# Kernel tuning notes

Measured on AMD Instinct MI355X. Metric: run time of the kernel, lower is better.

The kernel has to match this reference:

```python
import jax, jax.numpy as jnp
import numpy as np

B, L, D, H = 2, 2048, 1024, 16
Dh = D // H  # 64


def setup_inputs() -> dict:
    key = jax.random.key(0)
    ks = jax.random.split(key, 5)
    s_in = 1.0 / np.sqrt(D).astype(np.float32)
    s_out = 1.0 / np.sqrt(H * Dh).astype(np.float32)
    x = jax.random.normal(ks[0], (B, L, D), dtype=jnp.float32)
    Wq = jax.random.normal(ks[1], (D, H, Dh), dtype=jnp.float32) * s_in
    Wk = jax.random.normal(ks[2], (D, H, Dh), dtype=jnp.float32) * s_in
    Wv = jax.random.normal(ks[3], (D, H, Dh), dtype=jnp.float32) * s_in
    Wo = jax.random.normal(ks[4], (H, Dh, D), dtype=jnp.float32) * s_out
    bq = jnp.zeros((H, Dh), dtype=jnp.float32)
    bk = jnp.zeros((H, Dh), dtype=jnp.float32)
    bv = jnp.zeros((H, Dh), dtype=jnp.float32)
    bo = jnp.zeros((D,), dtype=jnp.float32)
    return {"x": x, "Wq": Wq, "bq": bq, "Wk": Wk, "bk": bk, "Wv": Wv, "bv": bv, "Wo": Wo, "bo": bo}


def reference(x, Wq, bq, Wk, bk, Wv, bv, Wo, bo):
    # QKV projections: LinearGeneral in_features=D -> (H, Dh), with bias
    q = jnp.einsum('bld,dhk->blhk', x, Wq) + bq  # [B,L,H,Dh]
    k = jnp.einsum('bld,dhk->blhk', x, Wk) + bk
    v = jnp.einsum('bld,dhk->blhk', x, Wv) + bv
    # NOTE: source uses FLOOR division for the scale (q // Dh**0.5) -- replicate exactly.
    q = q // (Dh ** 0.5)
    attn = jnp.einsum('blhk,bnhk->bhln', q, k)  # [B,H,L,L]
    causal = jnp.tril(jnp.ones((1, 1, L, L), dtype=jnp.float32))  # bidir=False -> pure causal
    neg_inf = jnp.finfo(jnp.float32).min
    attn = jnp.where(causal > 0, attn, neg_inf)
    attn = jax.nn.softmax(attn, axis=-1)
    o = jnp.einsum('bhln,bnhk->blhk', attn, v)  # [B,L,H,Dh]
    # Output projection: LinearGeneral (H, Dh) -> D over axes (-2,-1), with bias
    return jnp.einsum('blhk,hkd->bld', o, Wo) + bo
```

## Files before the change

kernel.cpp:

```cpp
#include <hip/hip_runtime.h>
#include <cstddef>
#include <cstdint>
#include <math.h>

typedef __bf16 bf16_t;
typedef __bf16 bf16x8 __attribute__((ext_vector_type(8)));
typedef float  f32x4  __attribute__((ext_vector_type(4)));

#define MFMA16(A,B,C) __builtin_amdgcn_mfma_f32_16x16x32_bf16((A),(B),(C),0,0,0)
#define QFIX_CAP 262144
#define QWIN 2e-3f


__device__ __forceinline__ void gload16(const bf16_t* g, bf16_t* l)
{
    auto* lp = reinterpret_cast<__attribute__((address_space(3))) uint32_t*>(
                   reinterpret_cast<uintptr_t>(l));
    const auto* gp = reinterpret_cast<const __attribute__((address_space(1))) uint32_t*>(
                   reinterpret_cast<uintptr_t>(g));
    __builtin_amdgcn_global_load_lds(gp, lp, 16, 0, 0);
}

__device__ __forceinline__ void gload4(const float* g, float* l)
{
    auto* lp = reinterpret_cast<__attribute__((address_space(3))) uint32_t*>(
                   reinterpret_cast<uintptr_t>(l));
    const auto* gp = reinterpret_cast<const __attribute__((address_space(1))) uint32_t*>(
                   reinterpret_cast<uintptr_t>(g));
    __builtin_amdgcn_global_load_lds(gp, lp, 4, 0, 0);
}

__global__ void k_conv_x(const float* __restrict__ x, bf16_t* __restrict__ xhi)
{
    int i = blockIdx.x * blockDim.x + threadIdx.x;
    float4 v = reinterpret_cast<const float4*>(x)[i];
    bf16_t* ph = xhi + 4*(size_t)i;
    ph[0]=(bf16_t)v.x; ph[1]=(bf16_t)v.y; ph[2]=(bf16_t)v.z; ph[3]=(bf16_t)v.w;
}

__global__ void k_transpose(const float* __restrict__ W, bf16_t* __restrict__ T)
{
    __shared__ float tile[32][33];
    int t = threadIdx.x, r = t >> 5, c = t & 31;
    int k0 = blockIdx.y * 32, n0 = blockIdx.x * 32;
#pragma unroll
    for (int i = 0; i < 4; i++)
        tile[r + i*8][c] = W[(size_t)(k0 + r + i*8) * 1024 + n0 + c];
    __syncthreads();
#pragma unroll
    for (int i = 0; i < 4; i++) {
        int nr = r + i*8;
        T[(size_t)(n0 + nr) * 1024 + k0 + c] = (bf16_t)tile[c][nr];
    }
}

__global__ void k_transpose_f32(const float* __restrict__ W, float* __restrict__ T)
{
    __shared__ float tile[32][33];
    int t = threadIdx.x, r = t >> 5, c = t & 31;
    int k0 = blockIdx.y * 32, n0 = blockIdx.x * 32;
#pragma unroll
    for (int i = 0; i < 4; i++)
        tile[r + i*8][c] = W[(size_t)(k0 + r + i*8) * 1024 + n0 + c];
    __syncthreads();
#pragma unroll
    for (int i = 0; i < 4; i++) {
        int nr = r + i*8;
        T[(size_t)(n0 + nr) * 1024 + k0 + c] = tile[c][nr];
    }
}

template<int MODE>
__launch_bounds__(256)
__global__ void k_gemm3(const bf16_t* __restrict__ A, const bf16_t* __restrict__ Bt,
                        const float* __restrict__ b0, const float* __restrict__ b1,
                        const float* __restrict__ b2,
                        bf16_t* __restrict__ qout, int2* __restrict__ qwl,
                        int* __restrict__ qcnt,
                        bf16_t* __restrict__ kho, bf16_t* __restrict__ vho,
                        float* __restrict__ fout)
{
    constexpr int BM = (MODE == 0) ? 128 : 64;
    __shared__ bf16_t As[3][BM*32]  __attribute__((aligned(16)));
    __shared__ bf16_t Bs[3][128*32] __attribute__((aligned(16)));

    const int bid = blockIdx.x;
    const int xcd = bid & 7;
    const int i   = bid >> 3;
    int n0, m0;
    if constexpr (MODE == 0) {
        n0 = (xcd * 3 + (i % 3)) * 128;
        m0 = (i / 3) * 128;
    } else {
        n0 = xcd * 128;
        m0 = i * 64;
    }

    const int tid = threadIdx.x;
    const int wid = tid >> 6, lane = tid & 63, lane16 = lane & 15, lg = lane >> 4;
    constexpr int WM = (MODE == 0) ? 64 : 32;
    const int wm = (wid >> 1) * WM, wn = (wid & 1) * 64;
    constexpr int MI = (MODE == 0) ? 4 : 2;

    f32x4 acc[MI][4] = {};

    auto STAGE = [&](int buf, int kt) {
        const int k0 = kt * 32;
#pragma unroll
        for (int i2 = 0; i2 < BM/64; i2++) {
            const int c = tid + i2*256;
            const int row = c >> 2, col = (c & 3) * 8;
            gload16(&A[(size_t)(m0 + row) * 1024 + k0 + col], &As[buf][c*8]);
        }
#pragma unroll
        for (int i2 = 0; i2 < 2; i2++) {
            const int c = tid + i2*256;
            const int row = c >> 2, col = (c & 3) * 8;
            gload16(&Bt[(size_t)(n0 + row) * 1024 + k0 + col], &Bs[buf][c*8]);
        }
    };

    STAGE(0, 0);
    STAGE(1, 1);
    for (int kt = 0; kt < 32; ++kt) {
        const int cur = kt % 3;
        if (kt < 31) {
            if constexpr (MODE == 0) { asm volatile("s_waitcnt vmcnt(4)" ::: "memory"); }
            else                     { asm volatile("s_waitcnt vmcnt(3)" ::: "memory"); }
        } else asm volatile("s_waitcnt vmcnt(0)" ::: "memory");
        __builtin_amdgcn_s_barrier();

        bf16x8 a[MI], b[4];
#pragma unroll
        for (int ii = 0; ii < MI; ii++)
            a[ii] = *reinterpret_cast<const bf16x8*>(&As[cur][(wm + ii*16 + lane16)*32 + lg*8]);
#pragma unroll
        for (int j = 0; j < 4; j++)
            b[j] = *reinterpret_cast<const bf16x8*>(&Bs[cur][(wn + j*16 + lane16)*32 + lg*8]);
#pragma unroll
        for (int ii = 0; ii < MI; ii++)
#pragma unroll
            for (int j = 0; j < 4; j++)
                acc[ii][j] = MFMA16(a[ii], b[j], acc[ii][j]);

        if (kt + 2 < 32) STAGE((kt + 2) % 3, kt + 2);
    }

    if constexpr (MODE == 1) {
#pragma unroll
        for (int j = 0; j < 4; j++) {
            const int n = n0 + wn + j*16 + lane16;
#pragma unroll
            for (int ii = 0; ii < MI; ii++)
#pragma unroll
                for (int r = 0; r < 4; r++) {
                    const int m = m0 + wm + ii*16 + lg*4 + r;
                    fout[(size_t)m*1024 + n] = acc[ii][j][r] + b0[n];
                }
        }
    } else if (n0 >= 1024) {
#pragma unroll
        for (int j = 0; j < 4; j++) {
            const int n = n0 + wn + j*16 + lane16;
#pragma unroll
            for (int ii = 0; ii < MI; ii++)
#pragma unroll
                for (int r = 0; r < 4; r++) {
                    const int m = m0 + wm + ii*16 + lg*4 + r;
                    const int bb = m >> 11, l = m & 2047;
                    float v = acc[ii][j][r];
                    if (n < 2048) {
                        const int nk = n - 1024;
                        kho[(((size_t)(bb*16 + (nk>>6)))*2048 + l)*64 + (nk&63)] =
                            (bf16_t)(v + b1[nk]);
                    } else {
                        const int nv = n - 2048;
                        vho[(((size_t)(bb*16 + (nv>>6)))*64 + (nv&63))*2048 + l] =
                            (bf16_t)(v + b2[nv]);
                    }
                }
        }
    } else {
        int cnt = 0;
#pragma unroll
        for (int j = 0; j < 4; j++) {
            const int n = n0 + wn + j*16 + lane16;
            const float bias = b0[n];
#pragma unroll
            for (int ii = 0; ii < MI; ii++)
#pragma unroll
                for (int r = 0; r < 4; r++) {
                    const int m = m0 + wm + ii*16 + lg*4 + r;
                    const int bb = m >> 11, l = m & 2047;
                    float t  = (acc[ii][j][r] + bias) * 0.125f;
                    float fl = floorf(t);
                    float fr = t - fl;
                    cnt += (fr < QWIN || fr > 1.0f - QWIN) ? 1 : 0;
                    qout[(((size_t)(bb*16 + (n>>6)))*2048 + l)*64 + (n&63)] = (bf16_t)fl;
                }
        }
        int pre = cnt;
#pragma unroll
        for (int off = 1; off < 64; off <<= 1) {
            int t2 = __shfl_up(pre, off);
            if (lane >= off) pre += t2;
        }
        int total = __shfl(pre, 63);
        int base = 0;
        if (lane == 63 && total > 0) base = atomicAdd(qcnt, total);
        base = __shfl(base, 63);
        int idx = base + pre - cnt;
#pragma unroll
        for (int j = 0; j < 4; j++) {
            const int n = n0 + wn + j*16 + lane16;
            const float bias = b0[n];
#pragma unroll
            for (int ii = 0; ii < MI; ii++)
#pragma unroll
                for (int r = 0; r < 4; r++) {
                    const int m = m0 + wm + ii*16 + lg*4 + r;
                    float t  = (acc[ii][j][r] + bias) * 0.125f;
                    float fr = t - floorf(t);
                    if (fr < QWIN || fr > 1.0f - QWIN) {
                        if (idx < QFIX_CAP) qwl[idx] = make_int2(m, n);
                        idx++;
                    }
                }
        }
    }
}

__launch_bounds__(64)
__global__ void k_qfix(const float* __restrict__ x, const float* __restrict__ WqT,
                       const float* __restrict__ bq, const int2* __restrict__ wl,
                       const int* __restrict__ count, bf16_t* __restrict__ qout)
{
    __shared__ float xs [64][65];
    __shared__ float wsd[64][65];
    int cnt = *count; if (cnt > QFIX_CAP) cnt = QFIX_CAP;
    const int base = blockIdx.x * 64;
    if (base >= cnt) return;
    const int lane = threadIdx.x;
    const int i = base + lane;
    const bool act = (i < cnt);
    const int2 e = wl[act ? i : base];
    const int m = e.x, n = e.y;

    float r0 = 0.f, r1 = 0.f;
#pragma unroll 1
    for (int c = 0; c < 16; ++c) {
        const int d0 = c * 64;
#pragma unroll 8
        for (int s = 0; s < 64; ++s) {
            int ms = __shfl(m, s);
            int ns = __shfl(n, s);
            gload4(&x  [(size_t)ms * 1024 + d0 + lane], &xs [s][0]);
            gload4(&WqT[(size_t)ns * 1024 + d0 + lane], &wsd[s][0]);
        }
        asm volatile("s_waitcnt vmcnt(0)" ::: "memory");
        float racc = (c < 8) ? r0 : r1;
#pragma unroll
        for (int d = 0; d < 64; ++d)
            racc = fmaf(xs[lane][d], wsd[lane][d], racc);
        if (c < 8) r0 = racc; else r1 = racc;
        asm volatile("s_waitcnt lgkmcnt(0)" ::: "memory");
    }
    if (act) {
        float acc = __fadd_rn(r0, r1);
        float q = floorf(__fmul_rn(__fadd_rn(acc, bq[n]), 0.125f));
        qout[(((size_t)((m>>11)*16 + (n>>6)))*2048 + (m&2047))*64 + (n&63)] = (bf16_t)q;
    }
}

__launch_bounds__(256)
__global__ void k_attn(const bf16_t* __restrict__ qf,
                       const bf16_t* __restrict__ khi,
                       const bf16_t* __restrict__ vhiT,
                       bf16_t* __restrict__ ohi)
{
    __shared__ bf16_t Kh[2][64*72] __attribute__((aligned(16)));
    __shared__ bf16_t Vh[2][64*72] __attribute__((aligned(16)));
    __shared__ bf16_t Ph[4*16*72]  __attribute__((aligned(16)));
    const int tid = threadIdx.x, wid = tid >> 6, lane = tid & 63;
    const int lane16 = lane & 15, lg = lane >> 4;
    const int bid = blockIdx.x;
    const int xcd = bid & 7;
    const int ib  = bid >> 3;
    const int bh  = xcd * 4 + (ib & 3);
    const int bx  = ib >> 2;
    const bf16_t* qb  = qf   + (size_t)bh * 2048 * 64;
    const bf16_t* khb = khi  + (size_t)bh * 2048 * 64;
    const bf16_t* vhb = vhiT + (size_t)bh * 64 * 2048;
    const int b = bh >> 4, h = bh & 15;
    const float L2E = 1.44269504088896f;

    bf16x8 kreg[2], vreg[2];
    auto ISSUE = [&](int t) {
        const int kv0 = t * 64;
#pragma unroll
        for (int i = 0; i < 2; i++) {
            int cc = tid + i*256, row = cc >> 3, col8 = (cc & 7) * 8;
            kreg[i] = *reinterpret_cast<const bf16x8*>(&khb[(size_t)(kv0+row)*64 + col8]);
            vreg[i] = *reinterpret_cast<const bf16x8*>(&vhb[(size_t)row*2048 + kv0 + col8]);
        }
    };
    auto WRITE = [&](int buf) {
#pragma unroll
        for (int i = 0; i < 2; i++) {
            int cc = tid + i*256, row = cc >> 3, col8 = (cc & 7) * 8;
            *reinterpret_cast<bf16x8*>(&Kh[buf][row*72 + col8]) = kreg[i];
            *reinterpret_cast<bf16x8*>(&Vh[buf][row*72 + col8]) = vreg[i];
        }
    };

#pragma unroll 1
    for (int pass = 0; pass < 2; pass++) {
        const int qt = pass ? (31 - bx) : bx;
        const int q0 = qt * 64;
        const int qrow16 = q0 + wid*16 + lane16;

        bf16x8 qfr0 = *reinterpret_cast<const bf16x8*>(&qb[(size_t)qrow16*64 + lg*8]);
        bf16x8 qfr1 = *reinterpret_cast<const bf16x8*>(&qb[(size_t)qrow16*64 + 32 + lg*8]);

        f32x4 acco[4] = {};
        float mrow = -1e30f;
        float lrow[4] = {0.f, 0.f, 0.f, 0.f};

        __syncthreads();
        ISSUE(0);
        WRITE(0);

        for (int t = 0; t <= qt; t++) {
            const int cur = t & 1;
            if (t < qt) ISSUE(t + 1);
            __syncthreads();

            f32x4 s[4] = {};
            __builtin_amdgcn_s_setprio(1);
#pragma unroll
            for (int st = 0; st < 4; st++) {
                const int ro = (st*16 + lane16)*72;
                bf16x8 kh0 = *reinterpret_cast<const bf16x8*>(&Kh[cur][ro + lg*8]);
                bf16x8 kh1 = *reinterpret_cast<const bf16x8*>(&Kh[cur][ro + 32 + lg*8]);
                s[st] = MFMA16(qfr0, kh0, s[st]);
                s[st] = MFMA16(qfr1, kh1, s[st]);
            }
            __builtin_amdgcn_s_setprio(0);
            if (t == qt) {
#pragma unroll
                for (int st = 0; st < 4; st++) {
                    int key = t*64 + st*16 + lane16;
#pragma unroll
                    for (int r = 0; r < 4; r++) {
                        int qr = q0 + wid*16 + lg*4 + r;
                        if (key > qr) s[st][r] = -1e30f;
                    }
                }
            }
            float gm = s[0][0];
#pragma unroll
            for (int st = 0; st < 4; st++)
#pragma unroll
                for (int r = 0; r < 4; r++) gm = fmaxf(gm, s[st][r]);
#pragma unroll
            for (int off = 1; off < 16; off <<= 1)
                gm = fmaxf(gm, __shfl_xor(gm, off));

            if (__any(gm > mrow)) {
                float mn = fmaxf(mrow, gm);
                float scl = exp2f((mrow - mn) * L2E);
                mrow = mn;
#pragma unroll
                for (int r = 0; r < 4; r++) lrow[r] *= scl;
#pragma unroll
                for (int nf = 0; nf < 4; nf++)
#pragma unroll
                    for (int r = 0; r < 4; r++) acco[nf][r] *= scl;
            }
#pragma unroll
            for (int st = 0; st < 4; st++) {
#pragma unroll
                for (int r = 0; r < 4; r++) {
                    float p = exp2f((s[st][r] - mrow) * L2E);
                    lrow[r] += p;
                    Ph[wid*16*72 + (lg*4 + r)*72 + st*16 + lane16] = (bf16_t)p;
                }
            }

            __builtin_amdgcn_s_setprio(1);
#pragma unroll
            for (int ks = 0; ks < 2; ks++) {
                bf16x8 phf = *reinterpret_cast<const bf16x8*>(&Ph[wid*16*72 + lane16*72 + ks*32 + lg*8]);
#pragma unroll
                for (int nf = 0; nf < 4; nf++) {
                    bf16x8 vh = *reinterpret_cast<const bf16x8*>(&Vh[cur][(nf*16 + lane16)*72 + ks*32 + lg*8]);
                    acco[nf] = MFMA16(phf, vh, acco[nf]);
                }
            }
            __builtin_amdgcn_s_setprio(0);

            if (t < qt) WRITE(cur ^ 1);
        }

#pragma unroll
        for (int off = 1; off < 16; off <<= 1)
#pragma unroll
            for (int r = 0; r < 4; r++) lrow[r] += __shfl_xor(lrow[r], off);

#pragma unroll
        for (int r = 0; r < 4; r++) {
            float inv = 1.0f / lrow[r];
            int qr = q0 + wid*16 + lg*4 + r;
            size_t base = ((size_t)(b*2048 + qr))*1024 + h*64;
#pragma unroll
            for (int nf = 0; nf < 4; nf++)
                ohi[base + nf*16 + lane16] = (bf16_t)(acco[nf][r] * inv);
        }
    }
}

extern "C" void kernel_launch(void* const* d_in, const int* in_sizes, int n_in,
                              void* d_out, int out_size, void* d_ws, size_t ws_size,
                              hipStream_t stream)
{
    const float* x  = (const float*)d_in[0];
    const float* Wq = (const float*)d_in[1];
    const float* bq = (const float*)d_in[2];
    const float* Wk = (const float*)d_in[3];
    const float* bk = (const float*)d_in[4];
    const float* Wv = (const float*)d_in[5];
    const float* bv = (const float*)d_in[6];
    const float* Wo = (const float*)d_in[7];
    const float* bo = (const float*)d_in[8];

    char* ws = (char*)d_ws;
    const size_t MB = (size_t)1 << 20;
    bf16_t* xhi    = (bf16_t*)(ws +  0*MB);
    bf16_t* WThi   = (bf16_t*)(ws +  8*MB);
    bf16_t* WoThi  = (bf16_t*)(ws + 14*MB);
    bf16_t* qbuf   = (bf16_t*)(ws + 16*MB);
    bf16_t* khibuf = (bf16_t*)(ws + 24*MB);
    bf16_t* vhiT   = (bf16_t*)(ws + 32*MB);
    bf16_t* ohibuf = (bf16_t*)(ws + 40*MB);
    int2*   qwl    = (int2*)  (ws + 48*MB);
    int*    qcnt   = (int*)   (ws + 50*MB);
    float*  WqTf   = (float*) (ws + 52*MB);

    hipMemsetAsync(qcnt, 0, 4, stream);
    k_conv_x<<<4096, 256, 0, stream>>>(x, xhi);
    dim3 tg(32, 32);
    k_transpose<<<tg, 256, 0, stream>>>(Wq, WThi);
    k_transpose<<<tg, 256, 0, stream>>>(Wk, WThi + (size_t)1024*1024);
    k_transpose<<<tg, 256, 0, stream>>>(Wv, WThi + (size_t)2048*1024);
    k_transpose<<<tg, 256, 0, stream>>>(Wo, WoThi);
    k_transpose_f32<<<tg, 256, 0, stream>>>(Wq, WqTf);

    k_gemm3<0><<<768, 256, 0, stream>>>(xhi, WThi, bq, bk, bv,
                                        qbuf, qwl, qcnt, khibuf, vhiT, nullptr);
    k_qfix<<<4096, 64, 0, stream>>>(x, WqTf, bq, qwl, qcnt, qbuf);
    k_attn<<<512, 256, 0, stream>>>(qbuf, khibuf, vhiT, ohibuf);
    k_gemm3<1><<<512, 256, 0, stream>>>(ohibuf, WoThi, bo, nullptr, nullptr,
                                        nullptr, nullptr, nullptr,
                                        nullptr, nullptr, (float*)d_out);
}
```

Before: 239.3 us.

## Switch GEMM to double-buffered BK=64 pipeline and 128-row output tiles

```diff
diff --git a/kernel.cpp b/kernel.cpp
--- a/kernel.cpp
+++ b/kernel.cpp
@@ -80,9 +80,8 @@
                         bf16_t* __restrict__ kho, bf16_t* __restrict__ vho,
                         float* __restrict__ fout)
 {
-    constexpr int BM = (MODE == 0) ? 128 : 64;
-    __shared__ bf16_t As[3][BM*32]  __attribute__((aligned(16)));
-    __shared__ bf16_t Bs[3][128*32] __attribute__((aligned(16)));
+    __shared__ bf16_t As[2][128*64] __attribute__((aligned(16)));
+    __shared__ bf16_t Bs[2][128*64] __attribute__((aligned(16)));
 
     const int bid = blockIdx.x;
     const int xcd = bid & 7;
@@ -93,57 +92,58 @@
         m0 = (i / 3) * 128;
     } else {
         n0 = xcd * 128;
-        m0 = i * 64;
+        m0 = i * 128;
     }
 
     const int tid = threadIdx.x;
     const int wid = tid >> 6, lane = tid & 63, lane16 = lane & 15, lg = lane >> 4;
-    constexpr int WM = (MODE == 0) ? 64 : 32;
-    const int wm = (wid >> 1) * WM, wn = (wid & 1) * 64;
-    constexpr int MI = (MODE == 0) ? 4 : 2;
-
-    f32x4 acc[MI][4] = {};
+    const int wm = (wid >> 1) * 64, wn = (wid & 1) * 64;
+
+    f32x4 acc[4][4] = {};
 
     auto STAGE = [&](int buf, int kt) {
-        const int k0 = kt * 32;
-#pragma unroll
-        for (int i2 = 0; i2 < BM/64; i2++) {
+        const int k0 = kt * 64;
+#pragma unroll
+        for (int i2 = 0; i2 < 4; i2++) {
             const int c = tid + i2*256;
-            const int row = c >> 2, col = (c & 3) * 8;
+            const int row = c >> 3, col = (c & 7) * 8;
             gload16(&A[(size_t)(m0 + row) * 1024 + k0 + col], &As[buf][c*8]);
         }
 #pragma unroll
-        for (int i2 = 0; i2 < 2; i2++) {
+        for (int i2 = 0; i2 < 4; i2++) {
             const int c = tid + i2*256;
-            const int row = c >> 2, col = (c & 3) * 8;
+            const int row = c >> 3, col = (c & 7) * 8;
             gload16(&Bt[(size_t)(n0 + row) * 1024 + k0 + col], &Bs[buf][c*8]);
         }
     };
 
     STAGE(0, 0);
-    STAGE(1, 1);
-    for (int kt = 0; kt < 32; ++kt) {
-        const int cur = kt % 3;
-        if (kt < 31) {
-            if constexpr (MODE == 0) { asm volatile("s_waitcnt vmcnt(4)" ::: "memory"); }
-            else                     { asm volatile("s_waitcnt vmcnt(3)" ::: "memory"); }
-        } else asm volatile("s_waitcnt vmcnt(0)" ::: "memory");
+    for (int kt = 0; kt < 16; ++kt) {
+        const int cur = kt & 1;
+        if (kt < 15) {
+            STAGE(cur ^ 1, kt + 1);
+            asm volatile("s_waitcnt vmcnt(8)" ::: "memory");
+        } else {
+            asm volatile("s_waitcnt vmcnt(0)" ::: "memory");
+        }
         __builtin_amdgcn_s_barrier();
 
-        bf16x8 a[MI], b[4];
-#pragma unroll
-        for (int ii = 0; ii < MI; ii++)
-            a[ii] = *reinterpret_cast<const bf16x8*>(&As[cur][(wm + ii*16 + lane16)*32 + lg*8]);
-#pragma unroll
-        for (int j = 0; j < 4; j++)
-            b[j] = *reinterpret_cast<const bf16x8*>(&Bs[cur][(wn + j*16 + lane16)*32 + lg*8]);
-#pragma unroll
-        for (int ii = 0; ii < MI; ii++)
+#pragma unroll
+        for (int kk = 0; kk < 2; kk++) {
+            bf16x8 a[4], b[4];
+#pragma unroll
+            for (int ii = 0; ii < 4; ii++)
+                a[ii] = *reinterpret_cast<const bf16x8*>(&As[cur][(wm + ii*16 + lane16)*64 + kk*32 + lg*8]);
 #pragma unroll
             for (int j = 0; j < 4; j++)
-                acc[ii][j] = MFMA16(a[ii], b[j], acc[ii][j]);
-
-        if (kt + 2 < 32) STAGE((kt + 2) % 3, kt + 2);
+                b[j] = *reinterpret_cast<const bf16x8*>(&Bs[cur][(wn + j*16 + lane16)*64 + kk*32 + lg*8]);
+#pragma unroll
+            for (int ii = 0; ii < 4; ii++)
+#pragma unroll
+                for (int j = 0; j < 4; j++)
+                    acc[ii][j] = MFMA16(a[ii], b[j], acc[ii][j]);
+        }
+        __builtin_amdgcn_s_barrier();
     }
 
     if constexpr (MODE == 1) {
@@ -151,7 +151,7 @@
         for (int j = 0; j < 4; j++) {
             const int n = n0 + wn + j*16 + lane16;
 #pragma unroll
-            for (int ii = 0; ii < MI; ii++)
+            for (int ii = 0; ii < 4; ii++)
 #pragma unroll
                 for (int r = 0; r < 4; r++) {
                     const int m = m0 + wm + ii*16 + lg*4 + r;
@@ -163,7 +163,7 @@
         for (int j = 0; j < 4; j++) {
             const int n = n0 + wn + j*16 + lane16;
 #pragma unroll
-            for (int ii = 0; ii < MI; ii++)
+            for (int ii = 0; ii < 4; ii++)
 #pragma unroll
                 for (int r = 0; r < 4; r++) {
                     const int m = m0 + wm + ii*16 + lg*4 + r;
@@ -187,7 +187,7 @@
             const int n = n0 + wn + j*16 + lane16;
             const float bias = b0[n];
 #pragma unroll
-            for (int ii = 0; ii < MI; ii++)
+            for (int ii = 0; ii < 4; ii++)
 #pragma unroll
                 for (int r = 0; r < 4; r++) {
                     const int m = m0 + wm + ii*16 + lg*4 + r;
@@ -215,7 +215,7 @@
             const int n = n0 + wn + j*16 + lane16;
             const float bias = b0[n];
 #pragma unroll
-            for (int ii = 0; ii < MI; ii++)
+            for (int ii = 0; ii < 4; ii++)
 #pragma unroll
                 for (int r = 0; r < 4; r++) {
                     const int m = m0 + wm + ii*16 + lg*4 + r;
@@ -459,7 +459,7 @@
                                         qbuf, qwl, qcnt, khibuf, vhiT, nullptr);
     k_qfix<<<4096, 64, 0, stream>>>(x, WqTf, bq, qwl, qcnt, qbuf);
     k_attn<<<512, 256, 0, stream>>>(qbuf, khibuf, vhiT, ohibuf);
-    k_gemm3<1><<<512, 256, 0, stream>>>(ohibuf, WoThi, bo, nullptr, nullptr,
+    k_gemm3<1><<<256, 256, 0, stream>>>(ohibuf, WoThi, bo, nullptr, nullptr,
                                         nullptr, nullptr, nullptr,
                                         nullptr, nullptr, (float*)d_out);
 }
```

Result: no change. 244.0 us (+2.0%).
